# Performance work log

Hardware: AMD Instinct MI355X
Metric: run time of the kernel (lower is better)

Reference implementation:

```python
import jax, jax.numpy as jnp
import numpy as np

B, SQ, SK = 4, 4096, 1024
HID, SATD = 640, 768
NUM_HEADS, HEAD_DIM = 10, 64
GEO_RATIO, ROPE_BASE = 1.0, 10000.0
LOSS_W = 0.05


def _ln(x, g, b):
    m = x.mean(-1, keepdims=True)
    v = ((x - m) ** 2).mean(-1, keepdims=True)
    return (x - m) / jnp.sqrt(v + 1e-5) * g + b


def _rope(t, xy):
    # t: [B,H,S,D], xy: [B,S,2] continuous coordinates.
    # Half the rotary channels encode x, half encode y.
    q = HEAD_DIM // 4
    inv = ROPE_BASE ** (-jnp.arange(q, dtype=t.dtype) / q)  # [q]
    ang = jnp.concatenate([xy[..., 0:1] * GEO_RATIO * inv,
                           xy[..., 1:2] * GEO_RATIO * inv], axis=-1)  # [B,S,D/2]
    cos = jnp.cos(ang)[:, None]  # [B,1,S,D/2]
    sin = jnp.sin(ang)[:, None]
    t1, t2 = t[..., : HEAD_DIM // 2], t[..., HEAD_DIM // 2:]
    return jnp.concatenate([t1 * cos - t2 * sin, t1 * sin + t2 * cos], axis=-1)


def setup_inputs() -> dict:
    key = jax.random.key(0)
    ks = jax.random.split(key, 16)
    s = 0.02
    return {
        'hidden_states': jax.random.normal(ks[0], (B, SQ, HID), jnp.float32),
        'sat_tokens': jax.random.normal(ks[1], (B, SK, SATD), jnp.float32),
        'sat_xy': jax.random.normal(ks[2], (B, SK, 2), jnp.float32) * 10.0,
        'front_bev_xy': jax.random.normal(ks[3], (B, SQ, 2), jnp.float32) * 10.0,
        'front_plucker': jax.random.normal(ks[4], (B, SQ, 6), jnp.float32),
        'valid_mask': jax.random.uniform(ks[5], (B, SQ), jnp.float32),
        'Wq': jax.random.normal(ks[6], (HID, HID), jnp.float32) * s,
        'bq': jnp.zeros((HID,), jnp.float32),
        'sat_ln_g': jnp.ones((SATD,), jnp.float32),
        'sat_ln_b': jnp.zeros((SATD,), jnp.float32),
        'Wk': jax.random.normal(ks[7], (SATD, HID), jnp.float32) * s,
        'bk': jnp.zeros((HID,), jnp.float32),
        'Wv': jax.random.normal(ks[8], (SATD, HID), jnp.float32) * s,
        'bv': jnp.zeros((HID,), jnp.float32),
        'Wp1': jax.random.normal(ks[9], (6, HID), jnp.float32) * s,
        'bp1': jnp.zeros((HID,), jnp.float32),
        'Wp2': jax.random.normal(ks[10], (HID, HID), jnp.float32) * s,
        'bp2': jnp.zeros((HID,), jnp.float32),
        'gate_ln_g': jnp.ones((HID,), jnp.float32),
        'gate_ln_b': jnp.zeros((HID,), jnp.float32),
        'Wg': jax.random.normal(ks[11], (HID, 1), jnp.float32) * s,
        'bg': jnp.full((1,), -1.0, jnp.float32),
    }


def reference(hidden_states, sat_tokens, sat_xy, front_bev_xy, front_plucker,
              valid_mask, Wq, bq, sat_ln_g, sat_ln_b, Wk, bk, Wv, bv,
              Wp1, bp1, Wp2, bp2, gate_ln_g, gate_ln_b, Wg, bg):
    b = hidden_states.shape[0]
    sn = _ln(sat_tokens, sat_ln_g, sat_ln_b)
    query = hidden_states @ Wq + bq                      # [B,SQ,HID]
    key = sn @ Wk + bk                                   # [B,SK,HID]
    value = sn @ Wv + bv
    q = query.reshape(b, -1, NUM_HEADS, HEAD_DIM).transpose(0, 2, 1, 3)
    k = key.reshape(b, -1, NUM_HEADS, HEAD_DIM).transpose(0, 2, 1, 3)
    v = value.reshape(b, -1, NUM_HEADS, HEAD_DIM).transpose(0, 2, 1, 3)
    q = _rope(q, front_bev_xy)
    k = _rope(k, sat_xy)
    logits = jnp.einsum('bhqd,bhkd->bhqk', q, k) / np.sqrt(HEAD_DIM)
    probs = jax.nn.softmax(logits.astype(jnp.float32), axis=-1).astype(q.dtype)
    out_h = jnp.einsum('bhqk,bhkd->bhqd', probs, v)
    out_h = out_h.transpose(0, 2, 1, 3).reshape(b, -1, HID)
    # plucker-conditioned gate
    pf = jax.nn.silu(front_plucker @ Wp1 + bp1) @ Wp2 + bp2
    gate_ctx = hidden_states + pf
    gate = jax.nn.sigmoid(_ln(gate_ctx, gate_ln_g, gate_ln_b) @ Wg + bg)  # [B,SQ,1]
    vm = (valid_mask > 0.5)
    out = out_h * gate * vm[..., None].astype(out_h.dtype)
    # auxiliary masked-mean confidence loss over invalid positions
    inv = (~vm).astype(gate.dtype)
    denom = jnp.maximum(inv.sum(), 1.0)
    loss = (gate[..., 0] * inv).sum() / denom * LOSS_W
    return out, loss
```

## Files before the change

kernel.cpp:

```cpp
#include <hip/hip_runtime.h>
#include <cstdint>
#include <cstddef>

#define B_    4
#define SQ_   4096
#define SK_   1024
#define HID_  640
#define SATD_ 768
#define NH_   10
#define HD_   64

typedef __bf16 bf16_t;
typedef __bf16 bf16x4 __attribute__((ext_vector_type(4)));
typedef __bf16 bf16x8 __attribute__((ext_vector_type(8)));
typedef float  f32x4  __attribute__((ext_vector_type(4)));
typedef unsigned short u16x8 __attribute__((ext_vector_type(8)));

static __device__ __forceinline__ unsigned short f2u(float f) {
  bf16_t b = (bf16_t)f;
  return __builtin_bit_cast(unsigned short, b);
}
static __device__ __forceinline__ float u2f(unsigned short u) {
  return (float)__builtin_bit_cast(bf16_t, u);
}
static __device__ __forceinline__ f32x4 mfma16(bf16x8 a, bf16x8 b, f32x4 c) {
  return __builtin_amdgcn_mfma_f32_16x16x32_bf16(a, b, c, 0, 0, 0);
}
static __device__ __forceinline__ void glds16(const unsigned short* g, unsigned short* l) {
  __builtin_amdgcn_global_load_lds((const __attribute__((address_space(1))) void*)g,
                                   (__attribute__((address_space(3))) void*)l, 16, 0, 0);
}

__global__ __launch_bounds__(256) void k_prep(const float* __restrict__ Wq,
                                              const float* __restrict__ Wk,
                                              const float* __restrict__ Wv,
                                              const float* __restrict__ Wp2,
                                              unsigned short* __restrict__ wqT,
                                              unsigned short* __restrict__ kvT,
                                              unsigned short* __restrict__ wp2T,
                                              const float* __restrict__ bk,
                                              const float* __restrict__ bv,
                                              float* __restrict__ bias_kv,
                                              const float* __restrict__ sat,
                                              const float* __restrict__ slg,
                                              const float* __restrict__ slb,
                                              unsigned short* __restrict__ sn,
                                              const float* __restrict__ plk,
                                              const float* __restrict__ Wp1,
                                              const float* __restrict__ bp1,
                                              unsigned short* __restrict__ pf1) {
  __shared__ unsigned short tile[64 * 65];
  __shared__ float sb[8];
  const int bx = blockIdx.x, t = threadIdx.x;

  if (bx < 480) {
    int seg = bx / 120, inner = bx % 120;
    const float* W; unsigned short* D; int K;
    if (seg == 0)      { W = Wq;  D = wqT;  K = 640; }
    else if (seg == 1) { W = Wk;  D = kvT;  K = 768; }
    else if (seg == 2) { W = Wv;  D = kvT + (size_t)640 * 768; K = 768; }
    else               { W = Wp2; D = wp2T; K = 640; }
    const int ktiles = K / 64;
    int kt = inner % ktiles, ntile = inner / ktiles;
    if (ntile >= 10) return;
    const int k0 = kt * 64, n0 = ntile * 64;
    const int r = t >> 3, c8 = (t & 7) * 8;
#pragma unroll
    for (int i = 0; i < 2; i++) {
      int row = r + i * 32;
      const float* wp = W + (size_t)(k0 + row) * HID_ + n0 + c8;
      float4 a0 = *(const float4*)wp, a1 = *(const float4*)(wp + 4);
      tile[(c8 + 0) * 65 + row] = f2u(a0.x);
      tile[(c8 + 1) * 65 + row] = f2u(a0.y);
      tile[(c8 + 2) * 65 + row] = f2u(a0.z);
      tile[(c8 + 3) * 65 + row] = f2u(a0.w);
      tile[(c8 + 4) * 65 + row] = f2u(a1.x);
      tile[(c8 + 5) * 65 + row] = f2u(a1.y);
      tile[(c8 + 6) * 65 + row] = f2u(a1.z);
      tile[(c8 + 7) * 65 + row] = f2u(a1.w);
    }
    __syncthreads();
#pragma unroll
    for (int i = 0; i < 2; i++) {
      int nl = r + i * 32;
      u16x8 o;
#pragma unroll
      for (int u = 0; u < 8; u++) o[u] = tile[nl * 65 + c8 + u];
      *(u16x8*)(D + (size_t)(n0 + nl) * K + k0 + c8) = o;
    }
  } else if (bx < 485) {
    int i = (bx - 480) * 256 + t;
    if (i < HID_) bias_kv[i] = bk[i];
    else if (i < 2 * HID_) bias_kv[i] = bv[i - HID_];
  } else if (bx < 4581) {
    int r = bx - 485;
    const float* xr = sat + (size_t)r * SATD_;
    float v0 = xr[t], v1 = xr[t + 256], v2 = xr[t + 512];
    float s = v0 + v1 + v2;
    float ss = v0 * v0 + v1 * v1 + v2 * v2;
    for (int o = 32; o; o >>= 1) { s += __shfl_xor(s, o); ss += __shfl_xor(ss, o); }
    if ((t & 63) == 0) { sb[t >> 6] = s; sb[4 + (t >> 6)] = ss; }
    __syncthreads();
    s  = sb[0] + sb[1] + sb[2] + sb[3];
    ss = sb[4] + sb[5] + sb[6] + sb[7];
    float m = s * (1.f / SATD_);
    float rstd = rsqrtf(ss * (1.f / SATD_) - m * m + 1e-5f);
    unsigned short* orow = sn + (size_t)r * SATD_;
    orow[t]       = f2u((v0 - m) * rstd * slg[t]       + slb[t]);
    orow[t + 256] = f2u((v1 - m) * rstd * slg[t + 256] + slb[t + 256]);
    orow[t + 512] = f2u((v2 - m) * rstd * slg[t + 512] + slb[t + 512]);
  } else {
    int i = (bx - 4581) * 256 + t;
    int r = i / 80, c8 = (i - r * 80) * 8;
    const float* p = plk + (size_t)r * 6;
    float pv[6];
#pragma unroll
    for (int j = 0; j < 6; j++) pv[j] = p[j];
    u16x8 o;
#pragma unroll
    for (int u = 0; u < 8; u++) {
      int c = c8 + u;
      float a = bp1[c];
#pragma unroll
      for (int j = 0; j < 6; j++) a += pv[j] * Wp1[j * HID_ + c];
      o[u] = f2u(a / (1.f + __expf(-a)));
    }
    *(u16x8*)&pf1[(size_t)r * HID_ + c8] = o;
  }
}

__global__ __launch_bounds__(256) void k_gemm3(const unsigned short* __restrict__ pf1,
                                               const float* __restrict__ hidden,
                                               const unsigned short* __restrict__ sn,
                                               const unsigned short* __restrict__ wp2T,
                                               const unsigned short* __restrict__ wqT,
                                               const unsigned short* __restrict__ kvT,
                                               const float* __restrict__ bp2,
                                               const float* __restrict__ bq,
                                               const float* __restrict__ bias_kv,
                                               unsigned short* __restrict__ pf2,
                                               unsigned short* __restrict__ q_lin,
                                               unsigned short* __restrict__ k_lin,
                                               unsigned short* __restrict__ vT,
                                               const float* __restrict__ bev_xy,
                                               const float* __restrict__ sat_xy) {
  __shared__ unsigned short As[2][128 * 32];
  __shared__ unsigned short Bs[2][128 * 32];
  const int z = blockIdx.z;
  const int bx = blockIdx.x;
  int bm, bn, K;
  const unsigned short* BT;
  const float* bias;
  if (z == 2) {
    if (bx >= 320) return;
    const int xcd = bx & 7, jj = bx >> 3;
    bm = ((jj / 10) * 8 + xcd) * 128;
    bn = (jj % 10) * 128;
    K = 768; BT = kvT; bias = bias_kv;
  } else {
    const int xcd = bx & 7, jj = bx >> 3;
    bm = ((jj / 5) * 8 + xcd) * 128;
    bn = (jj % 5) * 128;
    K = 640;
    BT = z ? wqT : wp2T;
    bias = z ? bq : bp2;
  }

  const int t = threadIdx.x, wv = t >> 6, lane = t & 63;
  const int lc = lane & 15, quad = lane >> 4;
  const int wm = (wv >> 1) * 64, wn = (wv & 1) * 64;
  f32x4 acc[4][4];
  f32x4 zero = {0.f, 0.f, 0.f, 0.f};
#pragma unroll
  for (int i = 0; i < 4; i++)
#pragma unroll
    for (int j = 0; j < 4; j++) acc[i][j] = zero;
  const int srow = wv * 32 + (lane >> 2);
  const int sc8 = (lane & 3) * 8;

  for (int k0 = 0; k0 < K; k0 += 64) {
    __syncthreads();
    if (z == 0) {
#pragma unroll
      for (int h2 = 0; h2 < 2; h2++)
#pragma unroll
        for (int i = 0; i < 2; i++)
          glds16(pf1 + (size_t)(bm + srow + i * 16) * K + k0 + h2 * 32 + sc8,
                 &As[h2][(wv * 32 + i * 16) * 32]);
    } else if (z == 2) {
#pragma unroll
      for (int h2 = 0; h2 < 2; h2++)
#pragma unroll
        for (int i = 0; i < 2; i++)
          glds16(sn + (size_t)(bm + srow + i * 16) * K + k0 + h2 * 32 + sc8,
                 &As[h2][(wv * 32 + i * 16) * 32]);
    } else {
      const int r4 = t >> 2, c4 = (t & 3) * 8;
#pragma unroll
      for (int h2 = 0; h2 < 2; h2++)
#pragma unroll
        for (int i = 0; i < 2; i++) {
          const float* ap = hidden + (size_t)(bm + r4 + i * 64) * K + k0 + h2 * 32 + c4;
          float4 a0 = *(const float4*)ap, a1 = *(const float4*)(ap + 4);
          u16x8 u = { f2u(a0.x), f2u(a0.y), f2u(a0.z), f2u(a0.w),
                      f2u(a1.x), f2u(a1.y), f2u(a1.z), f2u(a1.w) };
          *(u16x8*)&As[h2][(r4 + i * 64) * 32 + c4] = u;
        }
    }
#pragma unroll
    for (int h2 = 0; h2 < 2; h2++)
#pragma unroll
      for (int i = 0; i < 2; i++)
        glds16(BT + (size_t)(bn + srow + i * 16) * K + k0 + h2 * 32 + sc8,
               &Bs[h2][(wv * 32 + i * 16) * 32]);
    __syncthreads();
#pragma unroll
    for (int h2 = 0; h2 < 2; h2++) {
      bf16x8 af[4], bfr[4];
#pragma unroll
      for (int mt = 0; mt < 4; mt++) af[mt]  = *(const bf16x8*)&As[h2][(wm + mt * 16 + lc) * 32 + quad * 8];
#pragma unroll
      for (int nt = 0; nt < 4; nt++) bfr[nt] = *(const bf16x8*)&Bs[h2][(wn + nt * 16 + lc) * 32 + quad * 8];
#pragma unroll
      for (int mt = 0; mt < 4; mt++)
#pragma unroll
        for (int nt = 0; nt < 4; nt++) acc[mt][nt] = mfma16(af[mt], bfr[nt], acc[mt][nt]);
    }
  }

  float bsv[4];
#pragma unroll
  for (int nt = 0; nt < 4; nt++) bsv[nt] = bias[bn + wn + nt * 16 + lc];
  const float inv = __builtin_amdgcn_exp2f(-(float)lc * 0.8304820237218407f);

  if (z == 0) {
#pragma unroll
    for (int mt = 0; mt < 4; mt++) {
      int row = bm + wm + mt * 16 + quad * 4;
#pragma unroll
      for (int r = 0; r < 4; r++) {
        unsigned short* crow = pf2 + (size_t)(row + r) * HID_ + bn + wn + lc;
        crow[0]  = f2u(acc[mt][0][r] + bsv[0]);
        crow[16] = f2u(acc[mt][1][r] + bsv[1]);
        crow[32] = f2u(acc[mt][2][r] + bsv[2]);
        crow[48] = f2u(acc[mt][3][r] + bsv[3]);
      }
    }
  } else if (z == 1) {
    const float qscale = 0.18033688011112042f;
#pragma unroll
    for (int mt = 0; mt < 4; mt++) {
      int row = bm + wm + mt * 16 + quad * 4;
#pragma unroll
      for (int r = 0; r < 4; r++) {
        unsigned short* crow = q_lin + (size_t)(row + r) * HID_ + bn + wn + lc;
        float v0 = acc[mt][0][r] + bsv[0];
        float v1 = acc[mt][1][r] + bsv[1];
        float v2 = acc[mt][2][r] + bsv[2];
        float v3 = acc[mt][3][r] + bsv[3];
        float2 xy = *(const float2*)&bev_xy[(size_t)(row + r) * 2];
        float s0, c0, s1, c1;
        __sincosf(xy.x * inv, &s0, &c0);
        __sincosf(xy.y * inv, &s1, &c1);
        crow[0]  = f2u((v0 * c0 - v2 * s0) * qscale);
        crow[32] = f2u((v0 * s0 + v2 * c0) * qscale);
        crow[16] = f2u((v1 * c1 - v3 * s1) * qscale);
        crow[48] = f2u((v1 * s1 + v3 * c1) * qscale);
      }
    }
  } else if (bn < HID_) {
#pragma unroll
    for (int mt = 0; mt < 4; mt++) {
      int row = bm + wm + mt * 16 + quad * 4;
#pragma unroll
      for (int r = 0; r < 4; r++) {
        unsigned short* crow = k_lin + (size_t)(row + r) * HID_ + bn + wn + lc;
        float v0 = acc[mt][0][r] + bsv[0];
        float v1 = acc[mt][1][r] + bsv[1];
        float v2 = acc[mt][2][r] + bsv[2];
        float v3 = acc[mt][3][r] + bsv[3];
        float2 xy = *(const float2*)&sat_xy[(size_t)(row + r) * 2];
        float s0, c0, s1, c1;
        __sincosf(xy.x * inv, &s0, &c0);
        __sincosf(xy.y * inv, &s1, &c1);
        crow[0]  = f2u(v0 * c0 - v2 * s0);
        crow[32] = f2u(v0 * s0 + v2 * c0);
        crow[16] = f2u(v1 * c1 - v3 * s1);
        crow[48] = f2u(v1 * s1 + v3 * c1);
      }
    }
  } else {
#pragma unroll
    for (int mt = 0; mt < 4; mt++) {
      int row0 = bm + wm + mt * 16 + quad * 4;
      int bidx = row0 >> 10, key0 = row0 & 1023;
#pragma unroll
      for (int nt = 0; nt < 4; nt++) {
        int d = bn - HID_ + wn + nt * 16 + lc;
        bf16x4 v;
#pragma unroll
        for (int r = 0; r < 4; r++) v[r] = (bf16_t)(acc[mt][nt][r] + bsv[nt]);
        *(bf16x4*)(vT + ((size_t)(bidx * HID_ + d) << 10) + key0) = v;
      }
    }
  }
}

__global__ __launch_bounds__(256) void k_gate(const float* __restrict__ hid,
                                              const unsigned short* __restrict__ pf2,
                                              const float* __restrict__ g,
                                              const float* __restrict__ be,
                                              const float* __restrict__ Wg,
                                              const float* __restrict__ bg,
                                              const float* __restrict__ vm,
                                              float* __restrict__ gate_buf,
                                              float* __restrict__ lg_buf) {
  const int row = blockIdx.x * 4 + (threadIdx.x >> 6);
  const int lane = threadIdx.x & 63;
  const float* hr = hid + (size_t)row * HID_;
  const unsigned short* pr = pf2 + (size_t)row * HID_;
  float x[10];
  float s = 0.f, ss = 0.f;
#pragma unroll
  for (int u = 0; u < 10; u++) {
    int c = u * 64 + lane;
    float v = hr[c] + u2f(pr[c]);
    x[u] = v; s += v; ss += v * v;
  }
#pragma unroll
  for (int o = 32; o; o >>= 1) { s += __shfl_xor(s, o); ss += __shfl_xor(ss, o); }
  float m = s * (1.f / HID_);
  float rstd = rsqrtf(ss * (1.f / HID_) - m * m + 1e-5f);
  float d = 0.f;
#pragma unroll
  for (int u = 0; u < 10; u++) {
    int c = u * 64 + lane;
    d += ((x[u] - m) * rstd * g[c] + be[c]) * Wg[c];
  }
#pragma unroll
  for (int o = 32; o; o >>= 1) d += __shfl_xor(d, o);
  if (lane == 0) {
    float gate = 1.f / (1.f + __expf(-(d + bg[0])));
    float v = vm[row];
    gate_buf[row] = (v > 0.5f) ? gate : 0.f;
    lg_buf[row]   = (v > 0.5f) ? 0.f : gate;
  }
}

__global__ __launch_bounds__(256) void k_attn(const unsigned short* __restrict__ q_lin,
                                              const unsigned short* __restrict__ k_lin,
                                              const unsigned short* __restrict__ vT,
                                              const float* __restrict__ gate_buf,
                                              float* __restrict__ out) {
  __shared__ unsigned short Ks[64 * 72];
  __shared__ unsigned short Vt[64 * 72];
  __shared__ unsigned short Pt[4][32 * 72];
  const int qb = blockIdx.x * 128;
  const int bh = blockIdx.y;
  const int b = bh / NH_, h = bh - b * NH_;
  const int t = threadIdx.x, wv = t >> 6, lane = t & 63;
  const int lc = lane & 15, quad = lane >> 4;
  unsigned short* myPt = &Pt[wv][0];

  const unsigned short* qbase = q_lin + (size_t)(b * SQ_ + qb + wv * 32 + lc) * HID_ + h * HD_;
  bf16x8 qf[2][2];
#pragma unroll
  for (int g = 0; g < 2; g++) {
    qf[g][0] = *(const bf16x8*)(qbase + (size_t)g * 16 * HID_ + quad * 8);
    qf[g][1] = *(const bf16x8*)(qbase + (size_t)g * 16 * HID_ + 32 + quad * 8);
  }
  f32x4 zero = {0.f, 0.f, 0.f, 0.f};
  f32x4 O[2][4];
#pragma unroll
  for (int g = 0; g < 2; g++)
#pragma unroll
    for (int dt = 0; dt < 4; dt++) O[g][dt] = zero;
  float l_run[2] = {0.f, 0.f};

  const unsigned short* Kg = k_lin + (size_t)b * SK_ * HID_ + h * HD_;
  const unsigned short* Vg = vT + ((size_t)b * HID_ + h * HD_) * SK_;
  const int srow = t >> 3, scol = (t & 7) * 8;

  u16x8 kpre[2], vpre[2];
#pragma unroll
  for (int i = 0; i < 2; i++) {
    kpre[i] = *(const u16x8*)(Kg + (size_t)(srow + i * 32) * HID_ + scol);
    vpre[i] = *(const u16x8*)(Vg + (size_t)(srow + i * 32) * SK_ + scol);
  }

  for (int kc = 0; kc < SK_; kc += 64) {
    __syncthreads();
#pragma unroll
    for (int i = 0; i < 2; i++) {
      int row = srow + i * 32;
      *(u16x8*)&Ks[row * 72 + scol] = kpre[i];
      *(u16x8*)&Vt[row * 72 + scol] = vpre[i];
    }
    __syncthreads();
    if (kc + 64 < SK_) {
#pragma unroll
      for (int i = 0; i < 2; i++) {
        kpre[i] = *(const u16x8*)(Kg + (size_t)(kc + 64 + srow + i * 32) * HID_ + scol);
        vpre[i] = *(const u16x8*)(Vg + (size_t)(srow + i * 32) * SK_ + kc + 64 + scol);
      }
    }

    f32x4 ST[2][4];
#pragma unroll
    for (int kt = 0; kt < 4; kt++) {
      bf16x8 ka0 = *(const bf16x8*)&Ks[(kt * 16 + lc) * 72 + quad * 8];
      bf16x8 ka1 = *(const bf16x8*)&Ks[(kt * 16 + lc) * 72 + 32 + quad * 8];
#pragma unroll
      for (int g = 0; g < 2; g++)
        ST[g][kt] = mfma16(ka1, qf[g][1], mfma16(ka0, qf[g][0], zero));
    }
#pragma unroll
    for (int g = 0; g < 2; g++) {
      float rs = 0.f;
#pragma unroll
      for (int kt = 0; kt < 4; kt++) {
        bf16x4 pk;
#pragma unroll
        for (int r = 0; r < 4; r++) {
          float p = __builtin_amdgcn_exp2f(ST[g][kt][r]);
          rs += p;
          pk[r] = (bf16_t)p;
        }
        *(bf16x4*)&myPt[(g * 16 + lc) * 72 + kt * 16 + quad * 4] = pk;
      }
      rs += __shfl_xor(rs, 16);
      rs += __shfl_xor(rs, 32);
      l_run[g] += rs;
    }
#pragma unroll
    for (int ks = 0; ks < 2; ks++) {
      bf16x8 va[4];
#pragma unroll
      for (int dt = 0; dt < 4; dt++)
        va[dt] = *(const bf16x8*)&Vt[(dt * 16 + lc) * 72 + ks * 32 + quad * 8];
#pragma unroll
      for (int g = 0; g < 2; g++) {
        bf16x8 pb = *(const bf16x8*)&myPt[(g * 16 + lc) * 72 + ks * 32 + quad * 8];
#pragma unroll
        for (int dt = 0; dt < 4; dt++)
          O[g][dt] = mfma16(va[dt], pb, O[g][dt]);
      }
    }
  }

#pragma unroll
  for (int g = 0; g < 2; g++) {
    int rg = b * SQ_ + qb + wv * 32 + g * 16 + lc;
    float gv = gate_buf[rg] / l_run[g];
    float* orow = out + (size_t)rg * HID_ + h * HD_;
#pragma unroll
    for (int dt = 0; dt < 4; dt++) {
      f32x4 o4 = O[g][dt] * gv;
      *(f32x4*)&orow[dt * 16 + quad * 4] = o4;
    }
  }
}

__global__ __launch_bounds__(256) void k_loss(const float* __restrict__ lg,
                                              const float* __restrict__ vm,
                                              float* __restrict__ out_loss) {
  int t = threadIdx.x;
  float s = 0.f, cnt = 0.f;
  for (int i = t; i < B_ * SQ_; i += 256) {
    s += lg[i];
    cnt += (vm[i] > 0.5f) ? 0.f : 1.f;
  }
  __shared__ float sb[8];
  for (int o = 32; o; o >>= 1) { s += __shfl_xor(s, o); cnt += __shfl_xor(cnt, o); }
  if ((t & 63) == 0) { sb[t >> 6] = s; sb[4 + (t >> 6)] = cnt; }
  __syncthreads();
  if (t == 0) {
    s   = sb[0] + sb[1] + sb[2] + sb[3];
    cnt = sb[4] + sb[5] + sb[6] + sb[7];
    out_loss[0] = s / fmaxf(cnt, 1.f) * 0.05f;
  }
}

extern "C" void kernel_launch(void* const* d_in, const int* in_sizes, int n_in,
                              void* d_out, int out_size, void* d_ws, size_t ws_size,
                              hipStream_t stream) {
  (void)in_sizes; (void)n_in; (void)out_size; (void)ws_size;
  const float* hidden = (const float*)d_in[0];
  const float* sat    = (const float*)d_in[1];
  const float* sat_xy = (const float*)d_in[2];
  const float* bev_xy = (const float*)d_in[3];
  const float* plk    = (const float*)d_in[4];
  const float* vm     = (const float*)d_in[5];
  const float* Wq     = (const float*)d_in[6];
  const float* bq     = (const float*)d_in[7];
  const float* slg    = (const float*)d_in[8];
  const float* slb    = (const float*)d_in[9];
  const float* Wk     = (const float*)d_in[10];
  const float* bk     = (const float*)d_in[11];
  const float* Wv     = (const float*)d_in[12];
  const float* bv     = (const float*)d_in[13];
  const float* Wp1    = (const float*)d_in[14];
  const float* bp1    = (const float*)d_in[15];
  const float* Wp2    = (const float*)d_in[16];
  const float* bp2    = (const float*)d_in[17];
  const float* glg    = (const float*)d_in[18];
  const float* glb    = (const float*)d_in[19];
  const float* Wg     = (const float*)d_in[20];
  const float* bg     = (const float*)d_in[21];
  float* out = (float*)d_out;

  char* ws = (char*)d_ws;
  size_t off = 0;
  auto alloc = [&](size_t bytes) -> char* {
    char* p = ws + off;
    off += (bytes + 255) & ~(size_t)255;
    return p;
  };
  unsigned short* pf2   = (unsigned short*)d_out;
  unsigned short* pf1   = (unsigned short*)alloc((size_t)16384 * 640 * 2);
  unsigned short* q_lin = (unsigned short*)alloc((size_t)16384 * 640 * 2);
  unsigned short* k_lin = (unsigned short*)alloc((size_t)4096 * 640 * 2);
  unsigned short* vT    = (unsigned short*)alloc((size_t)B_ * HID_ * SK_ * 2);
  unsigned short* sn    = (unsigned short*)alloc((size_t)4096 * 768 * 2);
  unsigned short* wqT   = (unsigned short*)alloc((size_t)640 * 640 * 2);
  unsigned short* kvT   = (unsigned short*)alloc((size_t)1280 * 768 * 2);
  unsigned short* wp2T  = (unsigned short*)alloc((size_t)640 * 640 * 2);
  float* bias_kv  = (float*)alloc(1280 * 4);
  float* gate_buf = (float*)alloc(16384 * 4);
  float* lg_buf   = (float*)alloc(16384 * 4);

  k_prep<<<9701, 256, 0, stream>>>(Wq, Wk, Wv, Wp2, wqT, kvT, wp2T,
                                   bk, bv, bias_kv,
                                   sat, slg, slb, sn,
                                   plk, Wp1, bp1, pf1);

  {
    dim3 g(640, 1, 3);
    k_gemm3<<<g, 256, 0, stream>>>(pf1, hidden, sn, wp2T, wqT, kvT,
                                   bp2, bq, bias_kv,
                                   pf2, q_lin, k_lin, vT, bev_xy, sat_xy);
  }

  k_gate<<<4096, 256, 0, stream>>>(hidden, pf2, glg, glb, Wg, bg, vm, gate_buf, lg_buf);

  {
    dim3 g(SQ_ / 128, B_ * NH_);
    k_attn<<<g, 256, 0, stream>>>(q_lin, k_lin, vT, gate_buf, out);
  }
  k_loss<<<1, 256, 0, stream>>>(lg_buf, vm, out + (size_t)B_ * SQ_ * HID_);
}
```

Baseline: 309.1 us.

## Double-buffer GEMM K-loop, flatten grid, enlarge attention Q tile with swizzled LDS

The projection GEMM now uses a double-buffered 32-wide K loop that prefetches the next tile, including register prefetch of the fp32 hidden rows, while computing the current one. It also launches a flat 1600-block grid with no idle z=2 blocks. The attention kernel processes 256 queries per block (64 per wave), so each K/V tile is reused across more queries. K/V shared memory is XOR-swizzled instead of padded to avoid bank conflicts. The trade-offs are higher register pressure in attention, fewer attention blocks (640), and more barriers per K step in the GEMM.

```diff
diff --git a/kernel.cpp b/kernel.cpp
--- a/kernel.cpp
+++ b/kernel.cpp
@@ -146,26 +146,31 @@
                                                const float* __restrict__ sat_xy) {
   __shared__ unsigned short As[2][128 * 32];
   __shared__ unsigned short Bs[2][128 * 32];
-  const int z = blockIdx.z;
   const int bx = blockIdx.x;
+  int z, inner;
+  if (bx < 640)       { z = 0; inner = bx; }
+  else if (bx < 1280) { z = 1; inner = bx - 640; }
+  else                { z = 2; inner = bx - 1280; }
   int bm, bn, K;
   const unsigned short* BT;
+  const unsigned short* Abf = nullptr;
   const float* bias;
-  if (z == 2) {
-    if (bx >= 320) return;
-    const int xcd = bx & 7, jj = bx >> 3;
-    bm = ((jj / 10) * 8 + xcd) * 128;
-    bn = (jj % 10) * 128;
-    K = 768; BT = kvT; bias = bias_kv;
-  } else {
-    const int xcd = bx & 7, jj = bx >> 3;
-    bm = ((jj / 5) * 8 + xcd) * 128;
-    bn = (jj % 5) * 128;
-    K = 640;
-    BT = z ? wqT : wp2T;
-    bias = z ? bq : bp2;
-  }
-
+  {
+    const int xcd = inner & 7, jj = inner >> 3;
+    if (z == 2) {
+      bm = ((jj / 10) * 8 + xcd) * 128;
+      bn = (jj % 10) * 128;
+      K = 768; BT = kvT; bias = bias_kv; Abf = sn;
+    } else {
+      bm = ((jj / 5) * 8 + xcd) * 128;
+      bn = (jj % 5) * 128;
+      K = 640;
+      BT = z ? wqT : wp2T;
+      bias = z ? bq : bp2;
+      Abf = pf1;
+    }
+  }
+  const int n_iter = K / 32;
   const int t = threadIdx.x, wv = t >> 6, lane = t & 63;
   const int lc = lane & 15, quad = lane >> 4;
   const int wm = (wv >> 1) * 64, wn = (wv & 1) * 64;
@@ -175,57 +180,67 @@
   for (int i = 0; i < 4; i++)
 #pragma unroll
     for (int j = 0; j < 4; j++) acc[i][j] = zero;
-  const int srow = wv * 32 + (lane >> 2);
-  const int sc8 = (lane & 3) * 8;
-
-  for (int k0 = 0; k0 < K; k0 += 64) {
+  const int grow = wv * 32 + (lane >> 2);
+  const int gc8 = (lane & 3) * 8;
+  const int frow = t >> 2, fc8 = (t & 3) * 8;
+  float4 ar[2][2];
+
+  if (z != 1) {
+#pragma unroll
+    for (int i = 0; i < 2; i++)
+      glds16(Abf + (size_t)(bm + grow + i * 16) * K + gc8, &As[0][(wv * 32 + i * 16) * 32]);
+  } else {
+#pragma unroll
+    for (int i = 0; i < 2; i++) {
+      const float* ap = hidden + (size_t)(bm + frow + i * 64) * K + fc8;
+      ar[i][0] = *(const float4*)ap;
+      ar[i][1] = *(const float4*)(ap + 4);
+    }
+  }
+#pragma unroll
+  for (int i = 0; i < 2; i++)
+    glds16(BT + (size_t)(bn + grow + i * 16) * K + gc8, &Bs[0][(wv * 32 + i * 16) * 32]);
+
+  for (int ki = 0; ki < n_iter; ki++) {
+    const int cur = ki & 1;
+    const int k1 = (ki + 1) * 32;
+    if (z == 1) {
+#pragma unroll
+      for (int i = 0; i < 2; i++) {
+        u16x8 u = { f2u(ar[i][0].x), f2u(ar[i][0].y), f2u(ar[i][0].z), f2u(ar[i][0].w),
+                    f2u(ar[i][1].x), f2u(ar[i][1].y), f2u(ar[i][1].z), f2u(ar[i][1].w) };
+        *(u16x8*)&As[cur][(frow + i * 64) * 32 + fc8] = u;
+      }
+    }
     __syncthreads();
-    if (z == 0) {
-#pragma unroll
-      for (int h2 = 0; h2 < 2; h2++)
+    if (ki + 1 < n_iter) {
+      if (z != 1) {
 #pragma unroll
         for (int i = 0; i < 2; i++)
-          glds16(pf1 + (size_t)(bm + srow + i * 16) * K + k0 + h2 * 32 + sc8,
-                 &As[h2][(wv * 32 + i * 16) * 32]);
-    } else if (z == 2) {
-#pragma unroll
-      for (int h2 = 0; h2 < 2; h2++)
-#pragma unroll
-        for (int i = 0; i < 2; i++)
-          glds16(sn + (size_t)(bm + srow + i * 16) * K + k0 + h2 * 32 + sc8,
-                 &As[h2][(wv * 32 + i * 16) * 32]);
-    } else {
-      const int r4 = t >> 2, c4 = (t & 3) * 8;
-#pragma unroll
-      for (int h2 = 0; h2 < 2; h2++)
+          glds16(Abf + (size_t)(bm + grow + i * 16) * K + k1 + gc8,
+                 &As[1 - cur][(wv * 32 + i * 16) * 32]);
+      } else {
 #pragma unroll
         for (int i = 0; i < 2; i++) {
-          const float* ap = hidden + (size_t)(bm + r4 + i * 64) * K + k0 + h2 * 32 + c4;
-          float4 a0 = *(const float4*)ap, a1 = *(const float4*)(ap + 4);
-          u16x8 u = { f2u(a0.x), f2u(a0.y), f2u(a0.z), f2u(a0.w),
-                      f2u(a1.x), f2u(a1.y), f2u(a1.z), f2u(a1.w) };
-          *(u16x8*)&As[h2][(r4 + i * 64) * 32 + c4] = u;
+          const float* ap = hidden + (size_t)(bm + frow + i * 64) * K + k1 + fc8;
+          ar[i][0] = *(const float4*)ap;
+          ar[i][1] = *(const float4*)(ap + 4);
         }
-    }
-#pragma unroll
-    for (int h2 = 0; h2 < 2; h2++)
+      }
 #pragma unroll
       for (int i = 0; i < 2; i++)
-        glds16(BT + (size_t)(bn + srow + i * 16) * K + k0 + h2 * 32 + sc8,
-               &Bs[h2][(wv * 32 + i * 16) * 32]);
-    __syncthreads();
-#pragma unroll
-    for (int h2 = 0; h2 < 2; h2++) {
-      bf16x8 af[4], bfr[4];
-#pragma unroll
-      for (int mt = 0; mt < 4; mt++) af[mt]  = *(const bf16x8*)&As[h2][(wm + mt * 16 + lc) * 32 + quad * 8];
-#pragma unroll
-      for (int nt = 0; nt < 4; nt++) bfr[nt] = *(const bf16x8*)&Bs[h2][(wn + nt * 16 + lc) * 32 + quad * 8];
-#pragma unroll
-      for (int mt = 0; mt < 4; mt++)
-#pragma unroll
-        for (int nt = 0; nt < 4; nt++) acc[mt][nt] = mfma16(af[mt], bfr[nt], acc[mt][nt]);
-    }
+        glds16(BT + (size_t)(bn + grow + i * 16) * K + k1 + gc8,
+               &Bs[1 - cur][(wv * 32 + i * 16) * 32]);
+    }
+    bf16x8 af[4], bfr[4];
+#pragma unroll
+    for (int mt = 0; mt < 4; mt++) af[mt]  = *(const bf16x8*)&As[cur][(wm + mt * 16 + lc) * 32 + quad * 8];
+#pragma unroll
+    for (int nt = 0; nt < 4; nt++) bfr[nt] = *(const bf16x8*)&Bs[cur][(wn + nt * 16 + lc) * 32 + quad * 8];
+#pragma unroll
+    for (int mt = 0; mt < 4; mt++)
+#pragma unroll
+      for (int nt = 0; nt < 4; nt++) acc[mt][nt] = mfma16(af[mt], bfr[nt], acc[mt][nt]);
   }
 
   float bsv[4];
@@ -352,40 +367,40 @@
                                               const unsigned short* __restrict__ vT,
                                               const float* __restrict__ gate_buf,
                                               float* __restrict__ out) {
-  __shared__ unsigned short Ks[64 * 72];
-  __shared__ unsigned short Vt[64 * 72];
-  __shared__ unsigned short Pt[4][32 * 72];
-  const int qb = blockIdx.x * 128;
+  __shared__ unsigned short Ks[64 * 64];
+  __shared__ unsigned short Vt[64 * 64];
+  __shared__ unsigned short Pt[4][64 * 72];
+  const int qb = blockIdx.x * 256;
   const int bh = blockIdx.y;
   const int b = bh / NH_, h = bh - b * NH_;
   const int t = threadIdx.x, wv = t >> 6, lane = t & 63;
   const int lc = lane & 15, quad = lane >> 4;
   unsigned short* myPt = &Pt[wv][0];
 
-  const unsigned short* qbase = q_lin + (size_t)(b * SQ_ + qb + wv * 32 + lc) * HID_ + h * HD_;
-  bf16x8 qf[2][2];
-#pragma unroll
-  for (int g = 0; g < 2; g++) {
+  const unsigned short* qbase = q_lin + (size_t)(b * SQ_ + qb + wv * 64 + lc) * HID_ + h * HD_;
+  bf16x8 qf[4][2];
+#pragma unroll
+  for (int g = 0; g < 4; g++) {
     qf[g][0] = *(const bf16x8*)(qbase + (size_t)g * 16 * HID_ + quad * 8);
     qf[g][1] = *(const bf16x8*)(qbase + (size_t)g * 16 * HID_ + 32 + quad * 8);
   }
   f32x4 zero = {0.f, 0.f, 0.f, 0.f};
-  f32x4 O[2][4];
-#pragma unroll
-  for (int g = 0; g < 2; g++)
+  f32x4 O[4][4];
+#pragma unroll
+  for (int g = 0; g < 4; g++)
 #pragma unroll
     for (int dt = 0; dt < 4; dt++) O[g][dt] = zero;
-  float l_run[2] = {0.f, 0.f};
+  float l_run[4] = {0.f, 0.f, 0.f, 0.f};
 
   const unsigned short* Kg = k_lin + (size_t)b * SK_ * HID_ + h * HD_;
   const unsigned short* Vg = vT + ((size_t)b * HID_ + h * HD_) * SK_;
-  const int srow = t >> 3, scol = (t & 7) * 8;
+  const int srow = t >> 3, sc = t & 7;
 
   u16x8 kpre[2], vpre[2];
 #pragma unroll
   for (int i = 0; i < 2; i++) {
-    kpre[i] = *(const u16x8*)(Kg + (size_t)(srow + i * 32) * HID_ + scol);
-    vpre[i] = *(const u16x8*)(Vg + (size_t)(srow + i * 32) * SK_ + scol);
+    kpre[i] = *(const u16x8*)(Kg + (size_t)(srow + i * 32) * HID_ + sc * 8);
+    vpre[i] = *(const u16x8*)(Vg + (size_t)(srow + i * 32) * SK_ + sc * 8);
   }
 
   for (int kc = 0; kc < SK_; kc += 64) {
@@ -393,36 +408,36 @@
 #pragma unroll
     for (int i = 0; i < 2; i++) {
       int row = srow + i * 32;
-      *(u16x8*)&Ks[row * 72 + scol] = kpre[i];
-      *(u16x8*)&Vt[row * 72 + scol] = vpre[i];
+      int off = row * 64 + ((sc ^ (row & 7)) << 3);
+      *(u16x8*)&Ks[off] = kpre[i];
+      *(u16x8*)&Vt[off] = vpre[i];
     }
     __syncthreads();
     if (kc + 64 < SK_) {
 #pragma unroll
       for (int i = 0; i < 2; i++) {
-        kpre[i] = *(const u16x8*)(Kg + (size_t)(kc + 64 + srow + i * 32) * HID_ + scol);
-        vpre[i] = *(const u16x8*)(Vg + (size_t)(srow + i * 32) * SK_ + kc + 64 + scol);
-      }
-    }
-
-    f32x4 ST[2][4];
-#pragma unroll
-    for (int kt = 0; kt < 4; kt++) {
-      bf16x8 ka0 = *(const bf16x8*)&Ks[(kt * 16 + lc) * 72 + quad * 8];
-      bf16x8 ka1 = *(const bf16x8*)&Ks[(kt * 16 + lc) * 72 + 32 + quad * 8];
-#pragma unroll
-      for (int g = 0; g < 2; g++)
-        ST[g][kt] = mfma16(ka1, qf[g][1], mfma16(ka0, qf[g][0], zero));
-    }
-#pragma unroll
-    for (int g = 0; g < 2; g++) {
+        kpre[i] = *(const u16x8*)(Kg + (size_t)(kc + 64 + srow + i * 32) * HID_ + sc * 8);
+        vpre[i] = *(const u16x8*)(Vg + (size_t)(srow + i * 32) * SK_ + kc + 64 + sc * 8);
+      }
+    }
+
+#pragma unroll
+    for (int g = 0; g < 4; g++) {
+      f32x4 ST[4];
+#pragma unroll
+      for (int kt = 0; kt < 4; kt++) {
+        int key = kt * 16 + lc;
+        bf16x8 ka0 = *(const bf16x8*)&Ks[key * 64 + ((quad ^ (key & 7)) << 3)];
+        bf16x8 ka1 = *(const bf16x8*)&Ks[key * 64 + (((quad + 4) ^ (key & 7)) << 3)];
+        ST[kt] = mfma16(ka1, qf[g][1], mfma16(ka0, qf[g][0], zero));
+      }
       float rs = 0.f;
 #pragma unroll
       for (int kt = 0; kt < 4; kt++) {
         bf16x4 pk;
 #pragma unroll
         for (int r = 0; r < 4; r++) {
-          float p = __builtin_amdgcn_exp2f(ST[g][kt][r]);
+          float p = __builtin_amdgcn_exp2f(ST[kt][r]);
           rs += p;
           pk[r] = (bf16_t)p;
         }
@@ -436,10 +451,12 @@
     for (int ks = 0; ks < 2; ks++) {
       bf16x8 va[4];
 #pragma unroll
-      for (int dt = 0; dt < 4; dt++)
-        va[dt] = *(const bf16x8*)&Vt[(dt * 16 + lc) * 72 + ks * 32 + quad * 8];
-#pragma unroll
-      for (int g = 0; g < 2; g++) {
+      for (int dt = 0; dt < 4; dt++) {
+        int d = dt * 16 + lc;
+        va[dt] = *(const bf16x8*)&Vt[d * 64 + (((ks * 4 + quad) ^ (d & 7)) << 3)];
+      }
+#pragma unroll
+      for (int g = 0; g < 4; g++) {
         bf16x8 pb = *(const bf16x8*)&myPt[(g * 16 + lc) * 72 + ks * 32 + quad * 8];
 #pragma unroll
         for (int dt = 0; dt < 4; dt++)
@@ -449,8 +466,8 @@
   }
 
 #pragma unroll
-  for (int g = 0; g < 2; g++) {
-    int rg = b * SQ_ + qb + wv * 32 + g * 16 + lc;
+  for (int g = 0; g < 4; g++) {
+    int rg = b * SQ_ + qb + wv * 64 + g * 16 + lc;
     float gv = gate_buf[rg] / l_run[g];
     float* orow = out + (size_t)rg * HID_ + h * HD_;
 #pragma unroll
@@ -534,17 +551,14 @@
                                    sat, slg, slb, sn,
                                    plk, Wp1, bp1, pf1);
 
+  k_gemm3<<<1600, 256, 0, stream>>>(pf1, hidden, sn, wp2T, wqT, kvT,
+                                    bp2, bq, bias_kv,
+                                    pf2, q_lin, k_lin, vT, bev_xy, sat_xy);
+
+  k_gate<<<4096, 256, 0, stream>>>(hidden, pf2, glg, glb, Wg, bg, vm, gate_buf, lg_buf);
+
   {
-    dim3 g(640, 1, 3);
-    k_gemm3<<<g, 256, 0, stream>>>(pf1, hidden, sn, wp2T, wqT, kvT,
-                                   bp2, bq, bias_kv,
-                                   pf2, q_lin, k_lin, vT, bev_xy, sat_xy);
-  }
-
-  k_gate<<<4096, 256, 0, stream>>>(hidden, pf2, glg, glb, Wg, bg, vm, gate_buf, lg_buf);
-
-  {
-    dim3 g(SQ_ / 128, B_ * NH_);
+    dim3 g(SQ_ / 256, B_ * NH_);
     k_attn<<<g, 256, 0, stream>>>(q_lin, k_lin, vT, gate_buf, out);
   }
   k_loss<<<1, 256, 0, stream>>>(lg_buf, vm, out + (size_t)B_ * SQ_ * HID_);
```

Result: slower. 332.2 us (+7.5%).
